# Kernel tuning notes

Hardware: AMD Instinct MI355X
Metric: run time of the kernel (lower is better)

Reference implementation:

```python
import math
import jax, jax.numpy as jnp
import numpy as np


def _alibi_slopes(n):
    def pow2_slopes(n):
        start = 2.0 ** (-(2.0 ** (-(math.log2(n) - 3))))
        return [start * (start ** i) for i in range(n)]
    if math.log2(n).is_integer():
        return pow2_slopes(n)
    cp2 = 2 ** math.floor(math.log2(n))
    return pow2_slopes(cp2) + _alibi_slopes(2 * cp2)[0::2][: n - cp2]


NUM_HEADS = 16


def setup_inputs() -> dict:
    key = jax.random.key(0)
    ks = jax.random.split(key, 5)
    B, S, H = 2, 2048, 2048
    return {
        "hidden_states": jax.random.normal(ks[0], (B, S, H), jnp.float32),
        "w_qkv": jax.random.normal(ks[1], (H, 3 * H), jnp.float32) * (H ** -0.5),
        "b_qkv": jax.random.normal(ks[2], (3 * H,), jnp.float32) * 0.02,
        "w_proj": jax.random.normal(ks[3], (H, H), jnp.float32) * (H ** -0.5),
        "b_proj": jax.random.normal(ks[4], (H,), jnp.float32) * 0.02,
    }


def reference(hidden_states, w_qkv, b_qkv, w_proj, b_proj):
    B, S, H = hidden_states.shape
    nh = NUM_HEADS
    hd = H // nh
    scale = 1.0 / hd  # mup scale_qk_dot_by_d=True -> d^-1 (not d^-0.5)

    qkv = hidden_states @ w_qkv + b_qkv  # [B,S,3H]
    q, k, v = jnp.split(qkv, 3, axis=-1)
    q = q.reshape(B, S, nh, hd)
    k = k.reshape(B, S, nh, hd)
    v = v.reshape(B, S, nh, hd)

    scores = jnp.einsum("bqhd,bkhd->bhqk", q, k) * scale  # [B,nh,S,S]

    slopes = jnp.asarray(_alibi_slopes(nh), dtype=scores.dtype)  # [nh]
    pos = jnp.arange(S)
    rel = (pos[None, :] - pos[:, None]).astype(scores.dtype)  # j - i, <=0 in causal region
    bias = slopes[:, None, None] * rel[None, :, :]  # [nh,S,S]
    causal = pos[None, :] <= pos[:, None]  # [S,S]

    scores = jnp.where(causal[None, None], scores + bias[None], jnp.finfo(scores.dtype).min)
    attn = jax.nn.softmax(scores, axis=-1)

    out = jnp.einsum("bhqk,bkhd->bqhd", attn, v).reshape(B, S, H)
    return out @ w_proj + b_proj
```

## Files before the change

kernel.cpp:

```cpp
#include <hip/hip_runtime.h>
#include <hip/hip_bf16.h>

typedef short bf16x8 __attribute__((ext_vector_type(8)));
typedef float f32x4 __attribute__((ext_vector_type(4)));
typedef unsigned short ushort_t;

#define NH 16
#define HD 128
#define SEQ 2048
#define HID 2048
#define NQKV 6144
#define BATCH 2

__device__ __forceinline__ ushort_t f2bf(float x) {
    unsigned u = __builtin_bit_cast(unsigned, x);
    u = (u + 0x7fffu + ((u >> 16) & 1u)) >> 16;
    return (ushort_t)u;
}

__device__ __forceinline__ void gl2lds16(const ushort_t* g, ushort_t* l) {
    __builtin_amdgcn_global_load_lds(
        (__attribute__((address_space(1))) void*)(g),
        (__attribute__((address_space(3))) void*)(l), 16, 0, 0);
}

__global__ __launch_bounds__(256) void to_bf16(
    const float* __restrict__ x, ushort_t* __restrict__ y, int n8) {
    int i = blockIdx.x * 256 + threadIdx.x;
    if (i >= n8) return;
    float4 a0 = *(const float4*)(x + (size_t)i * 8);
    float4 a1 = *(const float4*)(x + (size_t)i * 8 + 4);
    union { ushort_t u[8]; uint4 v; } p;
    p.u[0]=f2bf(a0.x); p.u[1]=f2bf(a0.y); p.u[2]=f2bf(a0.z); p.u[3]=f2bf(a0.w);
    p.u[4]=f2bf(a1.x); p.u[5]=f2bf(a1.y); p.u[6]=f2bf(a1.z); p.u[7]=f2bf(a1.w);
    *(uint4*)(y + (size_t)i * 8) = p.v;
}

__global__ __launch_bounds__(256) void transpose_to_bf16(
    const float* __restrict__ w, ushort_t* __restrict__ wT, int K, int N) {
    __shared__ float tile[32][33];
    int nb = blockIdx.x * 32, kb = blockIdx.y * 32;
    int tx = threadIdx.x, ty = threadIdx.y;
#pragma unroll
    for (int i = 0; i < 4; ++i) {
        int k = kb + ty + i * 8;
        tile[ty + i * 8][tx] = w[(size_t)k * N + nb + tx];
    }
    __syncthreads();
#pragma unroll
    for (int i = 0; i < 4; ++i) {
        int n = nb + ty + i * 8;
        wT[(size_t)n * K + kb + tx] = f2bf(tile[tx][ty + i * 8]);
    }
}

#define GEMM_KLOOP(A_, BT_)                                                     \
    const int t = threadIdx.x;                                                  \
    const int w = t >> 6, lane = t & 63, lm = lane & 15, lq = lane >> 4;        \
    const int wm = (w >> 1) * 64, wn = (w & 1) * 64;                            \
    const int lrow = lane >> 3, lsw = (lane & 7) ^ lrow;                        \
    f32x4 acc[4][4] = {};                                                       \
    const ushort_t* gA = A_ + (size_t)(mb + w * 32 + lrow) * HID + lsw * 8;     \
    const ushort_t* gB = BT_ + (size_t)(nb + w * 32 + lrow) * HID + lsw * 8;    \
    for (int kb = 0; kb < HID; kb += 64) {                                      \
        __syncthreads();                                                        \
        _Pragma("unroll")                                                       \
        for (int c = 0; c < 4; ++c) {                                           \
            gl2lds16(gA + (size_t)c * 8 * HID + kb, At + (w * 256 + c * 64) * 8); \
            gl2lds16(gB + (size_t)c * 8 * HID + kb, Bt + (w * 256 + c * 64) * 8); \
        }                                                                       \
        __syncthreads();                                                        \
        _Pragma("unroll")                                                       \
        for (int kc = 0; kc < 2; ++kc) {                                        \
            const int slot = (kc * 4 + lq) ^ (lm & 7);                          \
            bf16x8 af[4], bfr[4];                                               \
            _Pragma("unroll")                                                   \
            for (int mt = 0; mt < 4; ++mt)                                      \
                af[mt] = ((const bf16x8*)At)[(wm + mt * 16 + lm) * 8 + slot];   \
            _Pragma("unroll")                                                   \
            for (int nt = 0; nt < 4; ++nt)                                      \
                bfr[nt] = ((const bf16x8*)Bt)[(wn + nt * 16 + lm) * 8 + slot];  \
            _Pragma("unroll")                                                   \
            for (int mt = 0; mt < 4; ++mt)                                      \
                _Pragma("unroll")                                               \
                for (int nt = 0; nt < 4; ++nt)                                  \
                    acc[mt][nt] = __builtin_amdgcn_mfma_f32_16x16x32_bf16(      \
                        af[mt], bfr[nt], acc[mt][nt], 0, 0, 0);                 \
        }                                                                       \
    }

__global__ __launch_bounds__(256) void gemm_qkv(
    const ushort_t* __restrict__ A, const ushort_t* __restrict__ BT,
    const float* __restrict__ bias,
    ushort_t* __restrict__ qbuf, ushort_t* __restrict__ kbuf,
    ushort_t* __restrict__ vTbuf) {
    __shared__ unsigned shbuf[128 * 68];
    ushort_t* At = (ushort_t*)shbuf;
    ushort_t* Bt = At + 128 * 64;
    const int mb = blockIdx.x * 128;
    const int nb = blockIdx.y * 128;
    GEMM_KLOOP(A, BT)

    const int sec = nb >> 11;
    if (sec < 2) {
#pragma unroll
        for (int mt = 0; mt < 4; ++mt)
#pragma unroll
            for (int nt = 0; nt < 4; ++nt)
#pragma unroll
                for (int r = 0; r < 4; ++r) {
                    int m = mb + wm + mt * 16 + lq * 4 + r;
                    int c = nb + wn + nt * 16 + lm;
                    float val = acc[mt][nt][r] + bias[c];
                    int h = (c >> 7) & 15;
                    int d = c & 127;
                    int b = m >> 11, s = m & 2047;
                    size_t bh = (size_t)(b * NH + h);
                    ushort_t* dst = (sec == 0) ? qbuf : kbuf;
                    dst[(bh * SEQ + s) * HD + d] = f2bf(val);
                }
    } else {
        __syncthreads();
        unsigned* T = shbuf;
#pragma unroll
        for (int mt = 0; mt < 4; ++mt)
#pragma unroll
            for (int nt = 0; nt < 4; ++nt) {
                const int cl = wn + nt * 16 + lm;
                const int ml = wm + mt * 16 + lq * 4;
                const float bb = bias[nb + cl];
#pragma unroll
                for (int r = 0; r < 4; r += 2) {
                    unsigned pk = (unsigned)f2bf(acc[mt][nt][r] + bb) |
                                  ((unsigned)f2bf(acc[mt][nt][r + 1] + bb) << 16);
                    T[cl * 68 + ((ml + r) >> 1)] = pk;
                }
            }
        __syncthreads();
        const int d = t & 127, sh = t >> 7;
        const int b = mb >> 11, sbase = mb & 2047;
        const int hv = (nb >> 7) - 32;
        ushort_t* vrow = vTbuf + ((size_t)(b * NH + hv) * HD + d) * SEQ + sbase + sh * 64;
#pragma unroll
        for (int i = 0; i < 8; ++i)
            *(uint4*)(vrow + i * 8) = *(const uint4*)&T[d * 68 + sh * 32 + i * 4];
    }
}

__global__ __launch_bounds__(256) void gemm_proj(
    const ushort_t* __restrict__ A, const ushort_t* __restrict__ BT,
    const float* __restrict__ bias, float* __restrict__ out) {
    __shared__ ushort_t Abuf[128 * 64];
    __shared__ ushort_t Bbuf[128 * 64];
    ushort_t* At = Abuf;
    ushort_t* Bt = Bbuf;
    const int mb = blockIdx.x * 128;
    const int nb = blockIdx.y * 128;
    GEMM_KLOOP(A, BT)
#pragma unroll
    for (int mt = 0; mt < 4; ++mt)
#pragma unroll
        for (int nt = 0; nt < 4; ++nt)
#pragma unroll
            for (int r = 0; r < 4; ++r) {
                int m = mb + wm + mt * 16 + lq * 4 + r;
                int c = nb + wn + nt * 16 + lm;
                out[(size_t)m * HID + c] = acc[mt][nt][r] + bias[c];
            }
}

__global__ __launch_bounds__(256) void attn_kernel(
    const ushort_t* __restrict__ qb, const ushort_t* __restrict__ kbuf,
    const ushort_t* __restrict__ vT, ushort_t* __restrict__ ob) {
    __shared__ ushort_t Ks[2][64 * 128];
    __shared__ ushort_t Vs[2][128 * 64];
    __shared__ ushort_t Ps[4][16 * 72];

    const int bid = blockIdx.x;
    const int x = bid & 7, g = bid >> 3;
    const int qt = 31 - (g >> 2);
    const int bh = ((g & 3) << 3) | x;
    const int qbase = qt * 64;
    const int t = threadIdx.x, w = t >> 6, lane = t & 63;
    const int lm = lane & 15, lq = lane >> 4;

    const ushort_t* Qg = qb + (size_t)bh * SEQ * HD;
    const ushort_t* Kg = kbuf + (size_t)bh * SEQ * HD;
    const ushort_t* Vg = vT + (size_t)bh * HD * SEQ;

    const float LOG2E = 1.44269504f;
    const int h = bh & 15;
    const float slope2 = exp2f(-0.5f * (float)(h + 1)) * LOG2E;
    const float scale2 = (1.0f / 128.0f) * LOG2E;

    const int qg = qbase + w * 16 + lm;

    bf16x8 qf[4];
#pragma unroll
    for (int kc = 0; kc < 4; ++kc) {
        uint4 qv = *(const uint4*)(Qg + (size_t)qg * HD + kc * 32 + lq * 8);
        qf[kc] = __builtin_bit_cast(bf16x8, qv);
    }

    float foff[4][4];
#pragma unroll
    for (int mt = 0; mt < 4; ++mt)
#pragma unroll
        for (int r = 0; r < 4; ++r)
            foff[mt][r] = slope2 * (float)(mt * 16 + lq * 4 + r);

    int koffs[4], voffs[4];
#pragma unroll
    for (int i = 0; i < 4; ++i) {
        int ci = i * 256 + t;
        int kr = ci >> 4, ks = ci & 15;
        int kcg = (ks & 8) | ((ks & 7) ^ (kr & 7));
        koffs[i] = kr * HD + kcg * 8;
        int vr = ci >> 3, vs = ci & 7;
        int vcg = vs ^ (vr & 7);
        voffs[i] = vr * SEQ + vcg * 8;
    }

#define ATTN_STAGE(KT, BUF)                                                   \
    {                                                                         \
        const ushort_t* Kt_ = Kg + (size_t)(KT) * 64 * HD;                    \
        const ushort_t* Vt_ = Vg + (size_t)(KT) * 64;                         \
        _Pragma("unroll")                                                     \
        for (int i = 0; i < 4; ++i) {                                         \
            gl2lds16(Kt_ + koffs[i], Ks[BUF] + (i * 256 + w * 64) * 8);       \
            gl2lds16(Vt_ + voffs[i], Vs[BUF] + (i * 256 + w * 64) * 8);       \
        }                                                                     \
    }

    float mrow = -1e30f, lrow = 0.0f;
    f32x4 O[8] = {};
    const int nkt = qt + 1;

    ATTN_STAGE(0, 0)
    __syncthreads();

    for (int kt = 0; kt < nkt; ++kt) {
        const int cur = kt & 1;
        if (kt + 1 < nkt) ATTN_STAGE(kt + 1, cur ^ 1)

        f32x4 sacc[4] = {};
        __builtin_amdgcn_s_setprio(1);
#pragma unroll
        for (int kc = 0; kc < 4; ++kc) {
            const int slot = ((kc * 4 + lq) & 8) | (((kc * 4 + lq) & 7) ^ (lm & 7));
#pragma unroll
            for (int mt = 0; mt < 4; ++mt) {
                bf16x8 bk = *(const bf16x8*)&Ks[cur][((mt * 16 + lm) * 16 + slot) * 8];
                sacc[mt] = __builtin_amdgcn_mfma_f32_16x16x32_bf16(bk, qf[kc], sacc[mt], 0, 0, 0);
            }
        }
        __builtin_amdgcn_s_setprio(0);

        const float sbase = slope2 * (float)(kt * 64 - qg);
        float sc[4][4];
        if (kt == qt) {
#pragma unroll
            for (int mt = 0; mt < 4; ++mt)
#pragma unroll
                for (int r = 0; r < 4; ++r) {
                    float s = sacc[mt][r] * scale2 + (sbase + foff[mt][r]);
                    sc[mt][r] = (kt * 64 + mt * 16 + lq * 4 + r <= qg) ? s : -3e38f;
                }
        } else {
#pragma unroll
            for (int mt = 0; mt < 4; ++mt)
#pragma unroll
                for (int r = 0; r < 4; ++r)
                    sc[mt][r] = sacc[mt][r] * scale2 + (sbase + foff[mt][r]);
        }

        float tm = sc[0][0];
#pragma unroll
        for (int mt = 0; mt < 4; ++mt)
#pragma unroll
            for (int r = 0; r < 4; ++r) tm = fmaxf(tm, sc[mt][r]);
        tm = fmaxf(tm, __shfl_xor(tm, 16));
        tm = fmaxf(tm, __shfl_xor(tm, 32));

        const bool noresc = __all(tm <= mrow + 8.0f) && (kt > 0);
        float mnew, alpha;
        if (noresc) {
            mnew = mrow;
            alpha = 1.0f;
        } else {
            mnew = fmaxf(mrow, tm);
            alpha = __builtin_amdgcn_exp2f(mrow - mnew);
        }
        mrow = mnew;

        float psum = 0.0f;
#pragma unroll
        for (int mt = 0; mt < 4; ++mt) {
            float p0 = __builtin_amdgcn_exp2f(sc[mt][0] - mnew);
            float p1 = __builtin_amdgcn_exp2f(sc[mt][1] - mnew);
            float p2 = __builtin_amdgcn_exp2f(sc[mt][2] - mnew);
            float p3 = __builtin_amdgcn_exp2f(sc[mt][3] - mnew);
            psum += (p0 + p1) + (p2 + p3);
            uint2 wv;
            wv.x = ((unsigned)f2bf(p1) << 16) | f2bf(p0);
            wv.y = ((unsigned)f2bf(p3) << 16) | f2bf(p2);
            *(uint2*)&Ps[w][lm * 72 + mt * 16 + lq * 4] = wv;
        }
        psum += __shfl_xor(psum, 16);
        psum += __shfl_xor(psum, 32);
        lrow = lrow * alpha + psum;

        if (!noresc) {
            float av[4];
#pragma unroll
            for (int r = 0; r < 4; ++r) av[r] = __shfl(alpha, lq * 4 + r);
#pragma unroll
            for (int nt = 0; nt < 8; ++nt)
#pragma unroll
                for (int r = 0; r < 4; ++r) O[nt][r] *= av[r];
        }

        asm volatile("s_waitcnt lgkmcnt(0)" ::: "memory");
        __builtin_amdgcn_s_setprio(1);
#pragma unroll
        for (int kc2 = 0; kc2 < 2; ++kc2) {
            bf16x8 ap = *(const bf16x8*)&Ps[w][lm * 72 + kc2 * 32 + lq * 8];
            const int slot = (kc2 * 4 + lq) ^ (lm & 7);
#pragma unroll
            for (int nt = 0; nt < 8; ++nt) {
                bf16x8 bv = *(const bf16x8*)&Vs[cur][((nt * 16 + lm) * 8 + slot) * 8];
                O[nt] = __builtin_amdgcn_mfma_f32_16x16x32_bf16(ap, bv, O[nt], 0, 0, 0);
            }
        }
        __builtin_amdgcn_s_setprio(0);

        __syncthreads();
    }

    float lb[4];
#pragma unroll
    for (int r = 0; r < 4; ++r)
        lb[r] = __builtin_amdgcn_rcpf(__shfl(lrow, lq * 4 + r));
    const int b = bh >> 4;
#pragma unroll
    for (int nt = 0; nt < 8; ++nt)
#pragma unroll
        for (int r = 0; r < 4; ++r) {
            int s = qbase + w * 16 + lq * 4 + r;
            int d = nt * 16 + lm;
            ob[((size_t)(b * SEQ + s)) * HID + h * HD + d] = f2bf(O[nt][r] * lb[r]);
        }
#undef ATTN_STAGE
}

extern "C" void kernel_launch(void* const* d_in, const int* in_sizes, int n_in,
                              void* d_out, int out_size, void* d_ws, size_t ws_size,
                              hipStream_t stream) {
    const float* hidden = (const float*)d_in[0];
    const float* w_qkv = (const float*)d_in[1];
    const float* b_qkv = (const float*)d_in[2];
    const float* w_proj = (const float*)d_in[3];
    const float* b_proj = (const float*)d_in[4];
    float* out = (float*)d_out;

    char* ws = (char*)d_ws;
    size_t off = 0;
    ushort_t* wqkvT = (ushort_t*)(ws + off); off += (size_t)NQKV * HID * 2;
    ushort_t* wprojT = (ushort_t*)(ws + off); off += (size_t)HID * HID * 2;
    ushort_t* hbf = (ushort_t*)(ws + off); off += (size_t)BATCH * SEQ * HID * 2;
    ushort_t* qw = (ushort_t*)(ws + off); off += (size_t)BATCH * NH * SEQ * HD * 2;
    ushort_t* kw = (ushort_t*)(ws + off); off += (size_t)BATCH * NH * SEQ * HD * 2;
    ushort_t* vTw = (ushort_t*)(ws + off); off += (size_t)BATCH * NH * SEQ * HD * 2;
    ushort_t* attnw = (ushort_t*)(ws + off); off += (size_t)BATCH * SEQ * HID * 2;

    to_bf16<<<dim3(BATCH * SEQ * HID / 8 / 256), 256, 0, stream>>>(
        hidden, hbf, BATCH * SEQ * HID / 8);
    transpose_to_bf16<<<dim3(NQKV / 32, HID / 32), dim3(32, 8), 0, stream>>>(
        w_qkv, wqkvT, HID, NQKV);
    transpose_to_bf16<<<dim3(HID / 32, HID / 32), dim3(32, 8), 0, stream>>>(
        w_proj, wprojT, HID, HID);

    gemm_qkv<<<dim3(BATCH * SEQ / 128, NQKV / 128), 256, 0, stream>>>(
        hbf, wqkvT, b_qkv, qw, kw, vTw);

    attn_kernel<<<dim3(BATCH * NH * 32), 256, 0, stream>>>(qw, kw, vTw, attnw);

    gemm_proj<<<dim3(BATCH * SEQ / 128, HID / 128), 256, 0, stream>>>(
        attnw, wprojT, b_proj, out);
}
```

Before: 364.4 us.

## Rewrite QKV GEMM as 256x256 tile with 8-wave pipelined LDS staging

```diff
diff --git a/kernel.cpp b/kernel.cpp
--- a/kernel.cpp
+++ b/kernel.cpp
@@ -89,61 +89,150 @@
         }                                                                       \
     }
 
-__global__ __launch_bounds__(256) void gemm_qkv(
+#define QSTAGE(GOP, OPIDX, SBUF, SKH, STILE)                                  \
+    _Pragma("unroll")                                                         \
+    for (int j = 0; j < 2; ++j)                                               \
+        gl2lds16(GOP + soff[j] + (STILE) * 64 + (SKH) * 32,                   \
+                 lds + (OPIDX) * 32768 + ((SBUF) * 2 + (SKH)) * 8192 +        \
+                     (j * 512 + w * 64) * 8);
+
+#define QLDA(BUF, KH)                                                         \
+    _Pragma("unroll")                                                         \
+    for (int mf = 0; mf < 8; ++mf) {                                          \
+        int rr = wm + mf * 16 + lm;                                           \
+        int slot = rr * 4 + (lq ^ ((rr >> 1) & 3));                           \
+        af[mf] = *(const bf16x8*)&lds[((BUF) * 2 + (KH)) * 8192 + slot * 8];  \
+    }
+
+#define QLDB(BUF, KH, NHALF)                                                  \
+    _Pragma("unroll")                                                         \
+    for (int nj = 0; nj < 2; ++nj) {                                          \
+        int rr = wn + ((NHALF) * 2 + nj) * 16 + lm;                           \
+        int slot = rr * 4 + (lq ^ ((rr >> 1) & 3));                           \
+        bfr[nj] = *(const bf16x8*)&lds[32768 + ((BUF) * 2 + (KH)) * 8192 + slot * 8]; \
+    }
+
+#define QPHASE(BUF, KH, NHALF, READA, GOP, OPIDX, SBUF, SKH, STILE, DRAIN)    \
+    QSTAGE(GOP, OPIDX, SBUF, SKH, STILE)                                      \
+    if (READA) { QLDA(BUF, KH) }                                              \
+    QLDB(BUF, KH, NHALF)                                                      \
+    asm volatile("" ::: "memory");                                            \
+    __builtin_amdgcn_s_barrier();                                             \
+    __builtin_amdgcn_sched_barrier(0);                                        \
+    __builtin_amdgcn_s_setprio(1);                                            \
+    _Pragma("unroll")                                                         \
+    for (int mf = 0; mf < 8; ++mf)                                            \
+        _Pragma("unroll")                                                     \
+        for (int nj = 0; nj < 2; ++nj)                                        \
+            acc[mf][(NHALF) * 2 + nj] = __builtin_amdgcn_mfma_f32_16x16x32_bf16( \
+                af[mf], bfr[nj], acc[mf][(NHALF) * 2 + nj], 0, 0, 0);         \
+    __builtin_amdgcn_s_setprio(0);                                            \
+    __builtin_amdgcn_sched_barrier(0);                                        \
+    if (DRAIN) { asm volatile("s_waitcnt vmcnt(8)" ::: "memory"); }           \
+    asm volatile("" ::: "memory");                                            \
+    __builtin_amdgcn_s_barrier();
+
+__global__ __launch_bounds__(512) void gemm_qkv(
     const ushort_t* __restrict__ A, const ushort_t* __restrict__ BT,
     const float* __restrict__ bias,
     ushort_t* __restrict__ qbuf, ushort_t* __restrict__ kbuf,
     ushort_t* __restrict__ vTbuf) {
-    __shared__ unsigned shbuf[128 * 68];
-    ushort_t* At = (ushort_t*)shbuf;
-    ushort_t* Bt = At + 128 * 64;
-    const int mb = blockIdx.x * 128;
-    const int nb = blockIdx.y * 128;
-    GEMM_KLOOP(A, BT)
+    __shared__ ushort_t lds[65536];
+    const int t = threadIdx.x;
+    const int w = t >> 6, lane = t & 63, lm = lane & 15, lq = lane >> 4;
+    const int wm = (w >> 2) * 128, wn = (w & 3) * 64;
+    const int mb = blockIdx.x * 256, nb = blockIdx.y * 256;
+
+    const ushort_t* gA = A + (size_t)mb * HID;
+    const ushort_t* gB = BT + (size_t)nb * HID;
+
+    int soff[2];
+#pragma unroll
+    for (int j = 0; j < 2; ++j) {
+        int r = j * 128 + (t >> 2);
+        int c = (t & 3) ^ ((r >> 1) & 3);
+        soff[j] = r * HID + c * 8;
+    }
+
+    f32x4 acc[8][4] = {};
+    bf16x8 af[8], bfr[2];
+
+    QSTAGE(gA, 0, 0, 0, 0) QSTAGE(gB, 1, 0, 0, 0)
+    QSTAGE(gA, 0, 0, 1, 0) QSTAGE(gB, 1, 0, 1, 0)
+    QSTAGE(gA, 0, 1, 0, 1) QSTAGE(gB, 1, 1, 0, 1)
+    asm volatile("s_waitcnt vmcnt(0)" ::: "memory");
+    __builtin_amdgcn_s_barrier();
+
+#pragma unroll 1
+    for (int i = 0; i < 16; ++i) {
+        const int Tb = 2 * i + 1;
+        const int T2 = (2 * i + 2) & 31, T3 = (2 * i + 3) & 31;
+        QPHASE(0, 0, 0, 1, gA, 0, 1, 1, Tb, 0)
+        QPHASE(0, 0, 1, 0, gB, 1, 1, 1, Tb, 1)
+        QPHASE(0, 1, 0, 1, gA, 0, 0, 0, T2, 0)
+        QPHASE(0, 1, 1, 0, gB, 1, 0, 0, T2, 1)
+        QPHASE(1, 0, 0, 1, gA, 0, 0, 1, T2, 0)
+        QPHASE(1, 0, 1, 0, gB, 1, 0, 1, T2, 1)
+        QPHASE(1, 1, 0, 1, gA, 0, 1, 0, T3, 0)
+        QPHASE(1, 1, 1, 0, gB, 1, 1, 0, T3, 1)
+    }
+
+    asm volatile("s_waitcnt vmcnt(0)" ::: "memory");
 
     const int sec = nb >> 11;
     if (sec < 2) {
 #pragma unroll
-        for (int mt = 0; mt < 4; ++mt)
-#pragma unroll
-            for (int nt = 0; nt < 4; ++nt)
+        for (int mf = 0; mf < 8; ++mf)
+#pragma unroll
+            for (int nf = 0; nf < 4; ++nf)
 #pragma unroll
                 for (int r = 0; r < 4; ++r) {
-                    int m = mb + wm + mt * 16 + lq * 4 + r;
-                    int c = nb + wn + nt * 16 + lm;
-                    float val = acc[mt][nt][r] + bias[c];
-                    int h = (c >> 7) & 15;
+                    int m = mb + wm + mf * 16 + lq * 4 + r;
+                    int c = nb + wn + nf * 16 + lm;
+                    float val = acc[mf][nf][r] + bias[c];
+                    int hh = (c >> 7) & 15;
                     int d = c & 127;
                     int b = m >> 11, s = m & 2047;
-                    size_t bh = (size_t)(b * NH + h);
+                    size_t bh = (size_t)(b * NH + hh);
                     ushort_t* dst = (sec == 0) ? qbuf : kbuf;
                     dst[(bh * SEQ + s) * HD + d] = f2bf(val);
                 }
     } else {
         __syncthreads();
-        unsigned* T = shbuf;
-#pragma unroll
-        for (int mt = 0; mt < 4; ++mt)
-#pragma unroll
-            for (int nt = 0; nt < 4; ++nt) {
-                const int cl = wn + nt * 16 + lm;
-                const int ml = wm + mt * 16 + lq * 4;
-                const float bb = bias[nb + cl];
-#pragma unroll
-                for (int r = 0; r < 4; r += 2) {
-                    unsigned pk = (unsigned)f2bf(acc[mt][nt][r] + bb) |
-                                  ((unsigned)f2bf(acc[mt][nt][r + 1] + bb) << 16);
-                    T[cl * 68 + ((ml + r) >> 1)] = pk;
+        unsigned* T = (unsigned*)lds;
+        const int b = mb >> 11, sbase = mb & 2047;
+        const int hv0 = (nb >> 7) - 32;
+        const int dd = t & 127, sh = t >> 7;
+#pragma unroll 1
+        for (int ch = 0; ch < 2; ++ch) {
+            if (((w >> 1) & 1) == ch) {
+                const int cl = (w & 1) * 64;
+#pragma unroll
+                for (int nf = 0; nf < 4; ++nf) {
+                    const int clc = cl + nf * 16 + lm;
+                    const float bb = bias[nb + ch * 128 + clc];
+#pragma unroll
+                    for (int mf = 0; mf < 8; ++mf) {
+                        const int ml = wm + mf * 16 + lq * 4;
+#pragma unroll
+                        for (int r = 0; r < 4; r += 2) {
+                            unsigned pk = (unsigned)f2bf(acc[mf][nf][r] + bb) |
+                                          ((unsigned)f2bf(acc[mf][nf][r + 1] + bb) << 16);
+                            T[clc * 132 + ((ml + r) >> 1)] = pk;
+                        }
+                    }
                 }
             }
-        __syncthreads();
-        const int d = t & 127, sh = t >> 7;
-        const int b = mb >> 11, sbase = mb & 2047;
-        const int hv = (nb >> 7) - 32;
-        ushort_t* vrow = vTbuf + ((size_t)(b * NH + hv) * HD + d) * SEQ + sbase + sh * 64;
-#pragma unroll
-        for (int i = 0; i < 8; ++i)
-            *(uint4*)(vrow + i * 8) = *(const uint4*)&T[d * 68 + sh * 32 + i * 4];
+            __syncthreads();
+            {
+                ushort_t* vrow = vTbuf +
+                    ((size_t)(b * NH + hv0 + ch) * HD + dd) * SEQ + sbase + sh * 64;
+#pragma unroll
+                for (int ii = 0; ii < 8; ++ii)
+                    *(uint4*)(vrow + ii * 8) = *(const uint4*)&T[dd * 132 + sh * 32 + ii * 4];
+            }
+            __syncthreads();
+        }
     }
 }
 
@@ -380,7 +469,7 @@
     transpose_to_bf16<<<dim3(HID / 32, HID / 32), dim3(32, 8), 0, stream>>>(
         w_proj, wprojT, HID, HID);
 
-    gemm_qkv<<<dim3(BATCH * SEQ / 128, NQKV / 128), 256, 0, stream>>>(
+    gemm_qkv<<<dim3(BATCH * SEQ / 256, NQKV / 256), 512, 0, stream>>>(
         hbf, wqkvT, b_qkv, qw, kw, vTw);
 
     attn_kernel<<<dim3(BATCH * NH * 32), 256, 0, stream>>>(qw, kw, vTw, attnw);
```

After: 377.3 us. 1.04x slower.
